# Kernel tuning notes

Measured on AMD Instinct MI355X. Metric: run time of the kernel, lower is better.

The kernel has to match this reference:

```python
import jax, jax.numpy as jnp
import numpy as np

WINDOW = 25
DIM_HEAD = 32


def _rel_pos_indices(w):
    # replicates the torch buffer: grid of (i,j) positions, pairwise offsets
    pos = np.arange(w)
    gi, gj = np.meshgrid(pos, pos, indexing='ij')
    grid = np.stack([gi.reshape(-1), gj.reshape(-1)], axis=-1)  # (w*w, 2)
    rel = grid[:, None, :] - grid[None, :, :] + (w - 1)          # (n, n, 2)
    return jnp.asarray(rel[..., 0] * (2 * w - 1) + rel[..., 1], dtype=jnp.int32)


def setup_inputs() -> dict:
    key = jax.random.key(0)
    k1, k2, k3, k4 = jax.random.split(key, 4)
    b, d, w = 32, 256, WINDOW
    heads = d // DIM_HEAD
    x = jax.random.normal(k1, (b, d, w, w), dtype=jnp.float32)
    W_qkv = jax.random.normal(k2, (d, 3 * d), dtype=jnp.float32) * 0.02
    W_out = jax.random.normal(k3, (d, d), dtype=jnp.float32) * 0.02
    rel_emb = jax.random.normal(k4, ((2 * w - 1) ** 2, heads), dtype=jnp.float32) * 0.02
    return {"x": x, "W_qkv": W_qkv, "W_out": W_out, "rel_emb": rel_emb}


def reference(x, W_qkv, W_out, rel_emb):
    b, d, H, W = x.shape
    h = d // DIM_HEAD
    scale = DIM_HEAD ** -0.5
    n = H * W

    # b d H W -> b n d
    xf = x.reshape(b, d, n).transpose(0, 2, 1)
    qkv = xf @ W_qkv                       # (b, n, 3d); columns ordered q,k,v
    q, k, v = jnp.split(qkv, 3, axis=-1)

    def to_heads(t):
        return t.reshape(b, n, h, DIM_HEAD).transpose(0, 2, 1, 3)  # b h n dh

    q = to_heads(q) * scale
    k = to_heads(k)
    v = to_heads(v)

    sim = jnp.einsum('bhid,bhjd->bhij', q, k)          # (b, h, n, n)
    bias = rel_emb[_rel_pos_indices(H)]                # (n, n, h)
    sim = sim + bias.transpose(2, 0, 1)[None]          # add per-head bias
    attn = jax.nn.softmax(sim, axis=-1)

    out = jnp.einsum('bhij,bhjd->bhid', attn, v)       # (b, h, n, dh)
    # b m (H W) dh -> b H W (m dh)  (head-major channel concat)
    out = out.transpose(0, 2, 1, 3).reshape(b, H, W, d)
    out = out @ W_out                                  # output projection (no bias)
    return out.transpose(0, 3, 1, 2)                   # b d H W
```

## Files before the change

### kernel.cpp

```cpp
#include <hip/hip_runtime.h>
#include <hip/hip_bf16.h>
#include <cstdint>

typedef __bf16 bf16x8 __attribute__((ext_vector_type(8)));
typedef __bf16 bf16x4 __attribute__((ext_vector_type(4)));
typedef float  f32x4  __attribute__((ext_vector_type(4)));

__device__ __forceinline__ int div25(int v) { return (v * 1311) >> 15; }

#if __has_builtin(__builtin_amdgcn_exp2f)
__device__ __forceinline__ float fast_exp2(float x) { return __builtin_amdgcn_exp2f(x); }
#else
__device__ __forceinline__ float fast_exp2(float x) { return exp2f(x); }
#endif

__device__ __forceinline__ void gll16(const __bf16* g, __bf16* l)
{
    __builtin_amdgcn_global_load_lds(
        (__attribute__((address_space(1))) void*)(g),
        (__attribute__((address_space(3))) void*)(l),
        16, 0, 0);
}

__device__ __forceinline__ int sniff_isbf(const void* p)
{
    const unsigned short* x = (const unsigned short*)p;
    int cnt = 0;
    #pragma unroll
    for (int i = 0; i < 16; ++i) {
        int e = (x[2 * i] >> 7) & 0xFF;
        cnt += (e >= 90 && e <= 143) ? 1 : 0;
    }
    return cnt > 8;
}

__global__ __launch_bounds__(256) void k_pre(
    const void* __restrict__ x, const void* __restrict__ Wqkv,
    const void* __restrict__ Wout, const void* __restrict__ rel,
    __bf16* __restrict__ xT, __bf16* __restrict__ Wt, __bf16* __restrict__ WoT,
    __bf16* __restrict__ biasC)
{
    __shared__ float tile[64][65];
    int bid = blockIdx.x;
    if (bid < 1280) {
        int isbf = sniff_isbf(x);
        int b = bid / 40, rem = bid % 40;
        int c0 = (rem % 10) * 64, r0 = (rem / 10) * 64;
        const int R = 256, C = 625, Cpad = 640;
        int tc = threadIdx.x & 63, tg = threadIdx.x >> 6;
        const unsigned short* sb = (const unsigned short*)x + (size_t)b * (256 * 625);
        const float*          sf = (const float*)x          + (size_t)b * (256 * 625);
        #pragma unroll
        for (int rr = 0; rr < 16; ++rr) {
            int r = r0 + tg * 16 + rr, c = c0 + tc;
            float v = 0.f;
            if (r < R && c < C) {
                if (isbf) v = __uint_as_float((unsigned int)sb[r * C + c] << 16);
                else      v = sf[r * C + c];
            }
            tile[tg * 16 + rr][tc] = v;
        }
        __syncthreads();
        __bf16* d = xT + (size_t)b * (640 * 256);
        #pragma unroll
        for (int rr = 0; rr < 16; ++rr) {
            int c = c0 + tg * 16 + rr, r = r0 + tc;
            if (c < Cpad && r < R) d[(size_t)c * R + r] = (__bf16)tile[tc][tg * 16 + rr];
        }
    } else if (bid < 1344) {
        int q = bid - 1280;
        int bx = q % 16, by = q / 16;
        int isbf = sniff_isbf(Wqkv);
        int isqkv = (bx < 12);
        int bxx = isqkv ? bx : (bx - 12);
        const void* src = isqkv ? Wqkv : Wout;
        __bf16* dst = isqkv ? Wt : WoT;
        int R = 256, C = isqkv ? 768 : 256;
        int r0 = by * 64, c0 = bxx * 64;
        int tc = threadIdx.x & 63, tg = threadIdx.x >> 6;
        const unsigned short* sb = (const unsigned short*)src;
        const float*          sf = (const float*)src;
        #pragma unroll
        for (int rr = 0; rr < 16; ++rr) {
            int r = r0 + tg * 16 + rr, c = c0 + tc;
            float v;
            if (isbf) v = __uint_as_float((unsigned int)sb[r * C + c] << 16);
            else      v = sf[r * C + c];
            tile[tg * 16 + rr][tc] = v;
        }
        __syncthreads();
        const float qs = 0.25503494f;
        #pragma unroll
        for (int rr = 0; rr < 16; ++rr) {
            int c = c0 + tg * 16 + rr, r = r0 + tc;
            float v = tile[tc][tg * 16 + rr];
            if (isqkv && c < 256) v *= qs;
            dst[(size_t)c * R + r] = (__bf16)v;
        }
    } else {
        const float LOG2E = 1.4426950408889634f;
        int isbf = sniff_isbf(rel);
        int q = bid - 1344;
        int ig = q % 40, h = q / 40;
        for (int t0 = 0; t0 < 10; ++t0) {
            int t  = t0 * 256 + threadIdx.x;
            int jc = t >> 7;
            int js = (t >> 6) & 1;
            int ln = t & 63;
            int qd = ln >> 4, l = ln & 15;
            int i = ig * 16 + l;
            int di = div25(i), ri = i - 25 * di;
            bf16x4 out;
            #pragma unroll
            for (int rr = 0; rr < 4; ++rr) {
                int j = jc * 32 + js * 16 + qd * 4 + rr;
                float v;
                if (j >= 625) {
                    v = -43281.f;
                } else {
                    int dj = div25(j);
                    int idx = (di - dj + 24) * 49 + ri - (j - 25 * dj) + 24;
                    idx = min(max(idx, 0), 2400);
                    float r;
                    if (isbf) r = (float)((const __bf16*)rel)[idx * 8 + h];
                    else      r = ((const float*)rel)[idx * 8 + h];
                    v = r * LOG2E;
                }
                out[rr] = (__bf16)v;
            }
            *(bf16x4*)(biasC + ((size_t)(h * 40 + ig) * 20 + jc) * 512 + ln * 8 + js * 4) = out;
        }
    }
}

#define AS(r, c) pool[(size_t)(r) * 32 + (c)]
#define BS(r, c) pool[4096 + (size_t)(r) * 32 + (c)]
#define CS(r, c) pool[(size_t)(r) * 44 + (c)]
__global__ __launch_bounds__(256, 2) void k_qkv(
    const __bf16* __restrict__ xT,
    const __bf16* __restrict__ Wt,
    __bf16* __restrict__ Q,
    __bf16* __restrict__ Km,
    __bf16* __restrict__ Vt)
{
    __shared__ __align__(16) __bf16 pool[8192];
    int L = blockIdx.x;
    int xcd = L & 7;
    int cc  = L >> 3;
    int pairIdx = xcd * 20 + cc / 6;
    int jt = cc - (cc / 6) * 6;
    int b  = pairIdx / 5;
    int pt = pairIdx - b * 5;
    int p0 = pt * 128, j0 = jt * 128;
    int tid = threadIdx.x;
    int w = tid >> 6, lane = tid & 63;
    int quad = lane >> 4, l15 = lane & 15;
    int wr = w >> 1, wc = w & 1;

    int srow = tid >> 2, scg = (tid & 3) * 8;
    const __bf16* ag  = xT + ((size_t)(b * 640 + p0 + srow) * 256) + scg;
    const __bf16* ag2 = ag + 64 * 256;
    const __bf16* bg  = Wt + ((size_t)(j0 + srow) * 256) + scg;
    const __bf16* bg2 = bg + 64 * 256;

    f32x4 acc[4][4] = {};
    for (int kk = 0; kk < 8; ++kk) {
        int c0 = kk * 32;
        __syncthreads();
        gll16(ag  + c0, &AS(srow, scg));
        gll16(ag2 + c0, &AS(64 + srow, scg));
        gll16(bg  + c0, &BS(srow, scg));
        gll16(bg2 + c0, &BS(64 + srow, scg));
        __syncthreads();
        bf16x8 af[4], bfr[4];
        #pragma unroll
        for (int t = 0; t < 4; ++t) {
            af[t]  = *(const bf16x8*)(&AS(wr * 64 + t * 16 + l15, quad * 8));
            bfr[t] = *(const bf16x8*)(&BS(wc * 64 + t * 16 + l15, quad * 8));
        }
        #pragma unroll
        for (int i = 0; i < 4; ++i)
            #pragma unroll
            for (int j = 0; j < 4; ++j)
                acc[i][j] = __builtin_amdgcn_mfma_f32_16x16x32_bf16(af[i], bfr[j], acc[i][j], 0, 0, 0);
    }

    if (jt < 4) {
        for (int r = 0; r < 4; ++r) {
            __syncthreads();
            if (wc == (r >> 1)) {
                #pragma unroll
                for (int i = 0; i < 4; ++i) {
                    #pragma unroll
                    for (int js = 0; js < 2; ++js) {
                        int jp = (r & 1) * 2 + js;
                        int col = js * 16 + l15;
                        int prow = wr * 64 + i * 16 + quad * 4;
                        #pragma unroll
                        for (int rr = 0; rr < 4; ++rr)
                            CS(prow + rr, col) = (__bf16)acc[i][jp][rr];
                    }
                }
            }
            __syncthreads();
            int jj = j0 + r * 32;
            __bf16* dst; int hh;
            if (jj < 256) { hh = jj >> 5; dst = Q; }
            else          { hh = (jj - 256) >> 5; dst = Km; }
            int p = tid >> 1, d0 = (tid & 1) * 16;
            size_t base = ((size_t)((b * 8 + hh) * 640) + p0 + p) * 32 + d0;
            #pragma unroll
            for (int k4 = 0; k4 < 4; ++k4) {
                bf16x4 v4 = *(const bf16x4*)(&CS(p, d0 + k4 * 4));
                *(bf16x4*)(dst + base + k4 * 4) = v4;
            }
        }
    } else {
        #pragma unroll
        for (int i = 0; i < 4; ++i) {
            #pragma unroll
            for (int j = 0; j < 4; ++j) {
                int jj = j0 + wc * 64 + j * 16 + l15 - 512;
                int h = jj >> 5, t = jj & 31;
                int p = p0 + wr * 64 + i * 16 + quad * 4;
                bf16x4 vv;
                #pragma unroll
                for (int rr = 0; rr < 4; ++rr) vv[rr] = (__bf16)acc[i][j][rr];
                *(bf16x4*)(Vt + ((size_t)((b * 8 + h) * 32) + t) * 640 + p) = vv;
            }
        }
    }
}

__global__ __launch_bounds__(128, 3) void k_attn(
    const __bf16* __restrict__ Q,
    const __bf16* __restrict__ Km,
    const __bf16* __restrict__ Vt,
    const __bf16* __restrict__ biasC,
    __bf16* __restrict__ ctx)
{
    __shared__ __align__(16) __bf16 P[2][2][64][44];
    __shared__ float ssum[2][64];
    int bh = blockIdx.x, b = bh >> 3, h = bh & 7;
    int tid = threadIdx.x, w = tid >> 6, lane = tid & 63;
    int quad = lane >> 4, l15 = lane & 15;
    int i0 = (blockIdx.y * 2 + w) * 64;

    bf16x8 qa[4];
    #pragma unroll
    for (int m = 0; m < 4; ++m)
        qa[m] = *(const bf16x8*)(Q + ((size_t)bh * 640 + i0 + 16 * m + l15) * 32 + quad * 8);
    const __bf16* kbase = Km + (size_t)bh * 640 * 32 + quad * 8;
    const __bf16* vbase = Vt + ((size_t)bh * 32 + l15) * 640 + quad * 8;
    const __bf16* bcb   = biasC + (size_t)(h * 40 + (i0 >> 4)) * 10240 + lane * 8;

    f32x4 o[4][2] = {};
    float psum[4] = {0.f, 0.f, 0.f, 0.f};

    bf16x8 k0 = *(const bf16x8*)(kbase + (size_t)l15 * 32);
    bf16x8 k1 = *(const bf16x8*)(kbase + (size_t)(16 + l15) * 32);
    bf16x8 bc[4];
    #pragma unroll
    for (int m = 0; m < 4; ++m)
        bc[m] = *(const bf16x8*)(bcb + m * 10240);
    bf16x8 vC0 = {}, vC1 = {};

    for (int c = 0; c < 20; ++c) {
        int buf = c & 1;
        f32x4 s[4][2];
        __builtin_amdgcn_s_setprio(1);
        #pragma unroll
        for (int m = 0; m < 4; ++m) {
            f32x4 f0, f1;
            #pragma unroll
            for (int rr = 0; rr < 4; ++rr) { f0[rr] = (float)bc[m][rr]; f1[rr] = (float)bc[m][4 + rr]; }
            s[m][0] = __builtin_amdgcn_mfma_f32_16x16x32_bf16(k0, qa[m], f0, 0, 0, 0);
            s[m][1] = __builtin_amdgcn_mfma_f32_16x16x32_bf16(k1, qa[m], f1, 0, 0, 0);
        }
        __builtin_amdgcn_s_setprio(0);
        int cn = min(c + 1, 19);
        bf16x8 k0n = *(const bf16x8*)(kbase + (size_t)(cn * 32 + l15) * 32);
        bf16x8 k1n = *(const bf16x8*)(kbase + (size_t)(cn * 32 + 16 + l15) * 32);
        bf16x8 vN0 = *(const bf16x8*)(vbase + c * 32);
        bf16x8 vN1 = *(const bf16x8*)(vbase + (size_t)16 * 640 + c * 32);
        bf16x8 bn[4];
        #pragma unroll
        for (int m = 0; m < 4; ++m)
            bn[m] = *(const bf16x8*)(bcb + m * 10240 + cn * 512);
        bf16x4 pk[4][2];
        #pragma unroll
        for (int m = 0; m < 4; ++m) {
            #pragma unroll
            for (int rr = 0; rr < 4; ++rr) {
                float e0 = fast_exp2(s[m][0][rr]); psum[m] += e0; pk[m][0][rr] = (__bf16)e0;
                float e1 = fast_exp2(s[m][1][rr]); psum[m] += e1; pk[m][1][rr] = (__bf16)e1;
            }
        }
        if (c > 0) {
            __builtin_amdgcn_s_setprio(1);
            #pragma unroll
            for (int m = 0; m < 4; ++m) {
                bf16x8 pa = *(const bf16x8*)(&P[w][buf ^ 1][16 * m + l15][quad * 8]);
                o[m][0] = __builtin_amdgcn_mfma_f32_16x16x32_bf16(pa, vC0, o[m][0], 0, 0, 0);
                o[m][1] = __builtin_amdgcn_mfma_f32_16x16x32_bf16(pa, vC1, o[m][1], 0, 0, 0);
            }
            __builtin_amdgcn_s_setprio(0);
        }
        #pragma unroll
        for (int m = 0; m < 4; ++m) {
            *(bf16x4*)(&P[w][buf][16 * m + l15][quad * 4])      = pk[m][0];
            *(bf16x4*)(&P[w][buf][16 * m + l15][16 + quad * 4]) = pk[m][1];
        }
        k0 = k0n; k1 = k1n; vC0 = vN0; vC1 = vN1;
        #pragma unroll
        for (int m = 0; m < 4; ++m) bc[m] = bn[m];
    }
    __builtin_amdgcn_s_setprio(1);
    #pragma unroll
    for (int m = 0; m < 4; ++m) {
        bf16x8 pa = *(const bf16x8*)(&P[w][1][16 * m + l15][quad * 8]);
        o[m][0] = __builtin_amdgcn_mfma_f32_16x16x32_bf16(pa, vC0, o[m][0], 0, 0, 0);
        o[m][1] = __builtin_amdgcn_mfma_f32_16x16x32_bf16(pa, vC1, o[m][1], 0, 0, 0);
    }
    __builtin_amdgcn_s_setprio(0);

    #pragma unroll
    for (int m = 0; m < 4; ++m) {
        psum[m] += __shfl_xor(psum[m], 16);
        psum[m] += __shfl_xor(psum[m], 32);
    }
    if (quad == 0)
        #pragma unroll
        for (int m = 0; m < 4; ++m) ssum[w][16 * m + l15] = psum[m];
    #pragma unroll
    for (int m = 0; m < 4; ++m) {
        #pragma unroll
        for (int rr = 0; rr < 4; ++rr) {
            int il = 16 * m + quad * 4 + rr;
            float inv = 1.f / ssum[w][il];
            size_t base = ((size_t)b * 640 + i0 + il) * 256 + h * 32;
            ctx[base + l15]      = (__bf16)(o[m][0][rr] * inv);
            ctx[base + 16 + l15] = (__bf16)(o[m][1][rr] * inv);
        }
    }
}

__global__ __launch_bounds__(256, 2) void k_outproj(
    const __bf16* __restrict__ ctx,
    const __bf16* __restrict__ WoT,
    const void* __restrict__ xorig,
    void* __restrict__ out)
{
    __shared__ __align__(16) __bf16 As2[64][40];
    __shared__ __align__(16) __bf16 Bs2[256][40];
    int isbf = sniff_isbf(xorig);
    int b = blockIdx.y, pt = blockIdx.x;
    int p0 = pt * 64;
    int tid = threadIdx.x, w = tid >> 6, lane = tid & 63;
    int quad = lane >> 4, l15 = lane & 15;
    int srow = tid >> 2, scg = (tid & 3) * 8;
    const __bf16* ag = ctx + ((size_t)(b * 640 + p0 + srow) * 256) + scg;
    const __bf16* bg = WoT + (size_t)srow * 256 + scg;

    f32x4 acc[4][4] = {};
    for (int kk = 0; kk < 8; ++kk) {
        int c0 = kk * 32;
        bf16x8 a0 = *(const bf16x8*)(ag + c0);
        bf16x8 b0 = *(const bf16x8*)(bg + c0);
        bf16x8 b1 = *(const bf16x8*)(bg + 64 * 256 + c0);
        bf16x8 b2 = *(const bf16x8*)(bg + 128 * 256 + c0);
        bf16x8 b3 = *(const bf16x8*)(bg + 192 * 256 + c0);
        __syncthreads();
        *(bf16x8*)(&As2[srow][scg])       = a0;
        *(bf16x8*)(&Bs2[srow][scg])       = b0;
        *(bf16x8*)(&Bs2[64 + srow][scg])  = b1;
        *(bf16x8*)(&Bs2[128 + srow][scg]) = b2;
        *(bf16x8*)(&Bs2[192 + srow][scg]) = b3;
        __syncthreads();
        bf16x8 af[4], bfr[4];
        #pragma unroll
        for (int t = 0; t < 4; ++t) {
            af[t]  = *(const bf16x8*)(&As2[t * 16 + l15][quad * 8]);
            bfr[t] = *(const bf16x8*)(&Bs2[w * 64 + t * 16 + l15][quad * 8]);
        }
        #pragma unroll
        for (int i = 0; i < 4; ++i)
            #pragma unroll
            for (int j = 0; j < 4; ++j)
                acc[i][j] = __builtin_amdgcn_mfma_f32_16x16x32_bf16(af[i], bfr[j], acc[i][j], 0, 0, 0);
    }
    __bf16* outb = (__bf16*)out;
    float*  outf = (float*)out;
    #pragma unroll
    for (int i = 0; i < 4; ++i) {
        #pragma unroll
        for (int j = 0; j < 4; ++j) {
            int co = w * 64 + j * 16 + l15;
            #pragma unroll
            for (int rr = 0; rr < 4; ++rr) {
                int p = p0 + i * 16 + quad * 4 + rr;
                if (p < 625) {
                    size_t o = ((size_t)(b * 256) + co) * 625 + p;
                    if (isbf) outb[o] = (__bf16)acc[i][j][rr];
                    else      outf[o] = acc[i][j][rr];
                }
            }
        }
    }
}

extern "C" void kernel_launch(void* const* d_in, const int* in_sizes, int n_in,
                              void* d_out, int out_size, void* d_ws, size_t ws_size,
                              hipStream_t stream)
{
    const void* x    = d_in[0];
    const void* Wqkv = d_in[1];
    const void* Wout = d_in[2];
    const void* rel  = d_in[3];

    __bf16* ws    = (__bf16*)d_ws;
    __bf16* xT    = ws;
    __bf16* Wt    = xT + 10485760;
    __bf16* WoT   = Wt + 196608;
    __bf16* Q     = WoT + 65536;
    __bf16* Km    = Q + 5242880;
    __bf16* Vt    = Km + 5242880;
    __bf16* biasC = Vt + 5242880;
    __bf16* ctx   = biasC + 3276800;

    k_pre<<<1664, 256, 0, stream>>>(x, Wqkv, Wout, rel, xT, Wt, WoT, biasC);
    k_qkv<<<dim3(960), 256, 0, stream>>>(xT, Wt, Q, Km, Vt);
    k_attn<<<dim3(256, 5), 128, 0, stream>>>(Q, Km, Vt, biasC, ctx);
    k_outproj<<<dim3(10, 32), 256, 0, stream>>>(ctx, WoT, x, d_out);
}
```

Before: 157.4 us.

## Double-buffer LDS tiles in QKV and out-projection GEMMs with async global-to-LDS loads

Both the QKV projection and output projection GEMM loops now use two LDS buffers. The next K-slice is prefetched with global_load_lds while MFMAs run on the current slice, which leaves one barrier per iteration instead of two. The out-projection also drops its register-staged global loads in favour of direct global-to-LDS copies. This doubles LDS use per block, which may reduce occupancy, and changes the padded layout to an unpadded 32-wide row, which can add bank conflicts.

```diff
diff --git a/kernel.cpp b/kernel.cpp
--- a/kernel.cpp
+++ b/kernel.cpp
@@ -133,9 +133,9 @@
     }
 }
 
-#define AS(r, c) pool[(size_t)(r) * 32 + (c)]
-#define BS(r, c) pool[4096 + (size_t)(r) * 32 + (c)]
-#define CS(r, c) pool[(size_t)(r) * 44 + (c)]
+#define AS(bf, r, c) pool[(size_t)(bf) * 8192 + (size_t)(r) * 32 + (c)]
+#define BS(bf, r, c) pool[(size_t)(bf) * 8192 + 4096 + (size_t)(r) * 32 + (c)]
+#define CS(r, c)     pool[(size_t)(r) * 44 + (c)]
 __global__ __launch_bounds__(256, 2) void k_qkv(
     const __bf16* __restrict__ xT,
     const __bf16* __restrict__ Wt,
@@ -143,7 +143,7 @@
     __bf16* __restrict__ Km,
     __bf16* __restrict__ Vt)
 {
-    __shared__ __align__(16) __bf16 pool[8192];
+    __shared__ __align__(16) __bf16 pool[16384];
     int L = blockIdx.x;
     int xcd = L & 7;
     int cc  = L >> 3;
@@ -163,26 +163,35 @@
     const __bf16* bg  = Wt + ((size_t)(j0 + srow) * 256) + scg;
     const __bf16* bg2 = bg + 64 * 256;
 
+    gll16(ag,  &AS(0, srow, scg));
+    gll16(ag2, &AS(0, 64 + srow, scg));
+    gll16(bg,  &BS(0, srow, scg));
+    gll16(bg2, &BS(0, 64 + srow, scg));
+    __syncthreads();
+
     f32x4 acc[4][4] = {};
     for (int kk = 0; kk < 8; ++kk) {
-        int c0 = kk * 32;
-        __syncthreads();
-        gll16(ag  + c0, &AS(srow, scg));
-        gll16(ag2 + c0, &AS(64 + srow, scg));
-        gll16(bg  + c0, &BS(srow, scg));
-        gll16(bg2 + c0, &BS(64 + srow, scg));
-        __syncthreads();
+        int cur = kk & 1;
+        if (kk < 7) {
+            int c0 = (kk + 1) * 32;
+            int nb = cur ^ 1;
+            gll16(ag  + c0, &AS(nb, srow, scg));
+            gll16(ag2 + c0, &AS(nb, 64 + srow, scg));
+            gll16(bg  + c0, &BS(nb, srow, scg));
+            gll16(bg2 + c0, &BS(nb, 64 + srow, scg));
+        }
         bf16x8 af[4], bfr[4];
         #pragma unroll
         for (int t = 0; t < 4; ++t) {
-            af[t]  = *(const bf16x8*)(&AS(wr * 64 + t * 16 + l15, quad * 8));
-            bfr[t] = *(const bf16x8*)(&BS(wc * 64 + t * 16 + l15, quad * 8));
+            af[t]  = *(const bf16x8*)(&AS(cur, wr * 64 + t * 16 + l15, quad * 8));
+            bfr[t] = *(const bf16x8*)(&BS(cur, wc * 64 + t * 16 + l15, quad * 8));
         }
         #pragma unroll
         for (int i = 0; i < 4; ++i)
             #pragma unroll
             for (int j = 0; j < 4; ++j)
                 acc[i][j] = __builtin_amdgcn_mfma_f32_16x16x32_bf16(af[i], bfr[j], acc[i][j], 0, 0, 0);
+        __syncthreads();
     }
 
     if (jt < 4) {
@@ -351,8 +360,7 @@
     const void* __restrict__ xorig,
     void* __restrict__ out)
 {
-    __shared__ __align__(16) __bf16 As2[64][40];
-    __shared__ __align__(16) __bf16 Bs2[256][40];
+    __shared__ __align__(16) __bf16 pool2[20480];
     int isbf = sniff_isbf(xorig);
     int b = blockIdx.y, pt = blockIdx.x;
     int p0 = pt * 64;
@@ -362,32 +370,38 @@
     const __bf16* ag = ctx + ((size_t)(b * 640 + p0 + srow) * 256) + scg;
     const __bf16* bg = WoT + (size_t)srow * 256 + scg;
 
+    gll16(ag,            &pool2[(size_t)srow * 32 + scg]);
+    gll16(bg,            &pool2[2048 + (size_t)srow * 32 + scg]);
+    gll16(bg + 64 * 256, &pool2[2048 + (size_t)(64 + srow) * 32 + scg]);
+    gll16(bg + 128 * 256,&pool2[2048 + (size_t)(128 + srow) * 32 + scg]);
+    gll16(bg + 192 * 256,&pool2[2048 + (size_t)(192 + srow) * 32 + scg]);
+    __syncthreads();
+
     f32x4 acc[4][4] = {};
     for (int kk = 0; kk < 8; ++kk) {
-        int c0 = kk * 32;
-        bf16x8 a0 = *(const bf16x8*)(ag + c0);
-        bf16x8 b0 = *(const bf16x8*)(bg + c0);
-        bf16x8 b1 = *(const bf16x8*)(bg + 64 * 256 + c0);
-        bf16x8 b2 = *(const bf16x8*)(bg + 128 * 256 + c0);
-        bf16x8 b3 = *(const bf16x8*)(bg + 192 * 256 + c0);
-        __syncthreads();
-        *(bf16x8*)(&As2[srow][scg])       = a0;
-        *(bf16x8*)(&Bs2[srow][scg])       = b0;
-        *(bf16x8*)(&Bs2[64 + srow][scg])  = b1;
-        *(bf16x8*)(&Bs2[128 + srow][scg]) = b2;
-        *(bf16x8*)(&Bs2[192 + srow][scg]) = b3;
-        __syncthreads();
+        int cur = kk & 1;
+        size_t base = (size_t)cur * 10240;
+        if (kk < 7) {
+            int c0 = (kk + 1) * 32;
+            size_t nb = (size_t)(cur ^ 1) * 10240;
+            gll16(ag + c0,             &pool2[nb + (size_t)srow * 32 + scg]);
+            gll16(bg + c0,             &pool2[nb + 2048 + (size_t)srow * 32 + scg]);
+            gll16(bg + 64 * 256 + c0,  &pool2[nb + 2048 + (size_t)(64 + srow) * 32 + scg]);
+            gll16(bg + 128 * 256 + c0, &pool2[nb + 2048 + (size_t)(128 + srow) * 32 + scg]);
+            gll16(bg + 192 * 256 + c0, &pool2[nb + 2048 + (size_t)(192 + srow) * 32 + scg]);
+        }
         bf16x8 af[4], bfr[4];
         #pragma unroll
         for (int t = 0; t < 4; ++t) {
-            af[t]  = *(const bf16x8*)(&As2[t * 16 + l15][quad * 8]);
-            bfr[t] = *(const bf16x8*)(&Bs2[w * 64 + t * 16 + l15][quad * 8]);
+            af[t]  = *(const bf16x8*)(&pool2[base + (size_t)(t * 16 + l15) * 32 + quad * 8]);
+            bfr[t] = *(const bf16x8*)(&pool2[base + 2048 + (size_t)(w * 64 + t * 16 + l15) * 32 + quad * 8]);
         }
         #pragma unroll
         for (int i = 0; i < 4; ++i)
             #pragma unroll
             for (int j = 0; j < 4; ++j)
                 acc[i][j] = __builtin_amdgcn_mfma_f32_16x16x32_bf16(af[i], bfr[j], acc[i][j], 0, 0, 0);
+        __syncthreads();
     }
     __bf16* outb = (__bf16*)out;
     float*  outf = (float*)out;
```

Result: no change. 155.4 us (-1.2%).
